# Kernel tuning notes

Measured on AMD Instinct MI355X. Metric: run time of the kernel, lower is better.

## Reference

```python
import jax, jax.numpy as jnp
import numpy as np

SCALE = 64.0
MARGIN = 0.35
EPS = 1e-7


def setup_inputs() -> dict:
    key = jax.random.key(0)
    k1, k2, k3 = jax.random.split(key, 3)
    B, D, C = 1024, 128, 100000
    embeddings = jax.random.normal(k1, (B, D), dtype=jnp.float32)
    labels = jax.random.randint(k2, (B,), 0, C, dtype=jnp.int64)
    W = jax.random.normal(k3, (C, D), dtype=jnp.float32)
    return {"embeddings": embeddings, "labels": labels, "W": W}


def reference(embeddings, labels, W):
    # L2-normalize class weights along feature dim (torch F.normalize, p=2, dim=1)
    W_norm = W / jnp.clip(jnp.linalg.norm(W, axis=1, keepdims=True), 1e-12)
    # cosine logits [B, C]
    cos_theta = jnp.clip(embeddings @ W_norm.T, -1.0 + EPS, 1.0 - EPS)
    # subtract margin only at the target class (equivalent to one-hot scatter)
    B = cos_theta.shape[0]
    rows = jnp.arange(B)
    cos_m = cos_theta.at[rows, labels].add(-MARGIN)
    logits = SCALE * cos_m
    # softmax cross-entropy with integer labels, mean reduction
    logp = jax.nn.log_softmax(logits, axis=-1)
    nll = -logp[rows, labels]
    return jnp.mean(nll)
```

## Files before the change

### kernel.cpp

```cpp
#include <hip/hip_runtime.h>
#include <hip/hip_bf16.h>

typedef __bf16 bf16x8 __attribute__((ext_vector_type(8)));
typedef float  f32x4  __attribute__((ext_vector_type(4)));

#define B_SZ 1024
#define D_SZ 128
#define C_SZ 100000
#define CPAD 100096
#define BM 128
#define BN 128
#define NG 64
#define NCT 782

#define SCALE_F   64.0f
#define MARGIN_F  0.35f
#define CLIP_F    (1.0f - 1e-7f)
#define LOG2E_F   1.4426950408889634f
#define S_LOG2E_F (64.0f * 1.4426950408889634f)

__device__ __forceinline__ void gload_lds16(const void* g, void* l) {
    __builtin_amdgcn_global_load_lds(
        (const __attribute__((address_space(1))) void*)g,
        (__attribute__((address_space(3))) void*)l, 16, 0, 0);
}

__global__ void norm_conv(const float* __restrict__ W, __bf16* __restrict__ Wb,
                          const float* __restrict__ E, __bf16* __restrict__ Eb) {
    const int b = blockIdx.x;
    if (b < 12512) {
        const int lane = threadIdx.x & 63;
        const int l32  = lane & 31;
        const int row  = b * 8 + ((threadIdx.x >> 6) << 1) + (lane >> 5);
        if (row < C_SZ) {
            float4 v = reinterpret_cast<const float4*>(W + (size_t)row * D_SZ)[l32];
            float ss = v.x * v.x + v.y * v.y + v.z * v.z + v.w * v.w;
            #pragma unroll
            for (int m = 1; m < 32; m <<= 1) ss += __shfl_xor(ss, m);
            float sc = 1.0f / fmaxf(sqrtf(ss), 1e-12f);
            union { __bf16 h[4]; uint2 u; } o;
            o.h[0] = (__bf16)(v.x * sc); o.h[1] = (__bf16)(v.y * sc);
            o.h[2] = (__bf16)(v.z * sc); o.h[3] = (__bf16)(v.w * sc);
            reinterpret_cast<uint2*>(Wb + (size_t)row * D_SZ)[l32] = o.u;
        } else {
            uint2 z; z.x = 0u; z.y = 0u;
            reinterpret_cast<uint2*>(Wb + (size_t)row * D_SZ)[l32] = z;
        }
    } else {
        const int i = (b - 12512) * 256 + threadIdx.x;
        float4 v = reinterpret_cast<const float4*>(E)[i];
        union { __bf16 h[4]; uint2 u; } o;
        o.h[0] = (__bf16)v.x; o.h[1] = (__bf16)v.y;
        o.h[2] = (__bf16)v.z; o.h[3] = (__bf16)v.w;
        reinterpret_cast<uint2*>(Eb)[i] = o.u;
    }
}

__launch_bounds__(512, 3)
__global__ void gemm_lse(const __bf16* __restrict__ Eb, const __bf16* __restrict__ Wb,
                         float* __restrict__ P) {
    __shared__ __bf16 sB[2][BN * D_SZ];
    __shared__ float  rs[2][BM];

    const int tid  = threadIdx.x;
    const int wave = tid >> 6;
    const int lane = tid & 63;
    const int g4   = lane >> 4;
    const int l15  = lane & 15;
    const int wm   = wave >> 1;
    const int wn   = wave & 1;
    const int g    = blockIdx.x;
    const int bi   = blockIdx.y;

    const int T = (NCT - g + NG - 1) / NG;

    const char* wbase = reinterpret_cast<const char*>(Wb);
    const int srcOff = ((tid >> 4) << 8) + ((((tid & 15) ^ ((tid >> 4) & 7))) << 4);
    const int ldsOff = wave << 10;

    {
        char* sb = reinterpret_cast<char*>(sB[0]);
        #pragma unroll
        for (int j = 0; j < 4; ++j)
            gload_lds16(wbase + (size_t)g * 32768 + j * 8192 + srcOff,
                        sb + j * 8192 + ldsOff);
    }

    bf16x8 a[2][4];
    {
        const char* ebase = reinterpret_cast<const char*>(Eb) + (size_t)bi * BM * 256;
        #pragma unroll
        for (int mi = 0; mi < 2; ++mi) {
            const char* pr = ebase + (wm * 32 + mi * 16 + l15) * 256 + g4 * 16;
            #pragma unroll
            for (int kk = 0; kk < 4; ++kk)
                a[mi][kk] = *reinterpret_cast<const bf16x8*>(pr + kk * 64);
        }
    }

    const int swz = (l15 & 7) << 4;
    int rowb[4];
    #pragma unroll
    for (int ni = 0; ni < 4; ++ni) rowb[ni] = (wn * 64 + ni * 16 + l15) * 256;
    int kb[4];
    #pragma unroll
    for (int kk = 0; kk < 4; ++kk) kb[kk] = (kk * 64 + g4 * 16) ^ swz;

    float rowsum[2][4] = {};

#define EPI(AC)                                                                  \
    _Pragma("unroll")                                                            \
    for (int mi = 0; mi < 2; ++mi) {                                             \
        _Pragma("unroll")                                                        \
        for (int r = 0; r < 4; ++r) {                                            \
            rowsum[mi][r] += __builtin_amdgcn_exp2f(                             \
                fminf(fmaf(AC[mi][0][r], S_LOG2E_F, -S_LOG2E_F), 0.0f));         \
            rowsum[mi][r] += __builtin_amdgcn_exp2f(                             \
                fminf(fmaf(AC[mi][1][r], S_LOG2E_F, -S_LOG2E_F), 0.0f));         \
        }                                                                        \
    }

    f32x4 acA[2][2], acB[2][2];
    #pragma unroll
    for (int mi = 0; mi < 2; ++mi)
        #pragma unroll
        for (int nh = 0; nh < 2; ++nh)
            acB[mi][nh] = (f32x4){0.f, 0.f, 0.f, 0.f};

    __syncthreads();

    int cur = 0;
    for (int t = 0; t < T; ++t) {
        if (t + 1 < T) {
            const size_t ci = (size_t)(g + (t + 1) * NG) * 32768;
            char* sb = reinterpret_cast<char*>(sB[cur ^ 1]);
            #pragma unroll
            for (int j = 0; j < 4; ++j)
                gload_lds16(wbase + ci + j * 8192 + srcOff, sb + j * 8192 + ldsOff);
        }

        const char* sBb = reinterpret_cast<const char*>(sB[cur]);

        __builtin_amdgcn_s_setprio(1);
        #pragma unroll
        for (int mi = 0; mi < 2; ++mi)
            #pragma unroll
            for (int nh = 0; nh < 2; ++nh)
                acA[mi][nh] = (f32x4){0.f, 0.f, 0.f, 0.f};
        #pragma unroll
        for (int kk = 0; kk < 4; ++kk) {
            bf16x8 b0 = *reinterpret_cast<const bf16x8*>(sBb + rowb[0] + kb[kk]);
            bf16x8 b1 = *reinterpret_cast<const bf16x8*>(sBb + rowb[1] + kb[kk]);
            acA[0][0] = __builtin_amdgcn_mfma_f32_16x16x32_bf16(a[0][kk], b0, acA[0][0], 0, 0, 0);
            acA[1][0] = __builtin_amdgcn_mfma_f32_16x16x32_bf16(a[1][kk], b0, acA[1][0], 0, 0, 0);
            acA[0][1] = __builtin_amdgcn_mfma_f32_16x16x32_bf16(a[0][kk], b1, acA[0][1], 0, 0, 0);
            acA[1][1] = __builtin_amdgcn_mfma_f32_16x16x32_bf16(a[1][kk], b1, acA[1][1], 0, 0, 0);
        }
        __builtin_amdgcn_s_setprio(0);
        EPI(acB);

        __builtin_amdgcn_s_setprio(1);
        #pragma unroll
        for (int mi = 0; mi < 2; ++mi)
            #pragma unroll
            for (int nh = 0; nh < 2; ++nh)
                acB[mi][nh] = (f32x4){0.f, 0.f, 0.f, 0.f};
        #pragma unroll
        for (int kk = 0; kk < 4; ++kk) {
            bf16x8 b2 = *reinterpret_cast<const bf16x8*>(sBb + rowb[2] + kb[kk]);
            bf16x8 b3 = *reinterpret_cast<const bf16x8*>(sBb + rowb[3] + kb[kk]);
            acB[0][0] = __builtin_amdgcn_mfma_f32_16x16x32_bf16(a[0][kk], b2, acB[0][0], 0, 0, 0);
            acB[1][0] = __builtin_amdgcn_mfma_f32_16x16x32_bf16(a[1][kk], b2, acB[1][0], 0, 0, 0);
            acB[0][1] = __builtin_amdgcn_mfma_f32_16x16x32_bf16(a[0][kk], b3, acB[0][1], 0, 0, 0);
            acB[1][1] = __builtin_amdgcn_mfma_f32_16x16x32_bf16(a[1][kk], b3, acB[1][1], 0, 0, 0);
        }
        __builtin_amdgcn_s_setprio(0);
        EPI(acA);

        __syncthreads();
        cur ^= 1;
    }
    EPI(acB);

    #pragma unroll
    for (int mi = 0; mi < 2; ++mi) {
        #pragma unroll
        for (int r = 0; r < 4; ++r) {
            float s = rowsum[mi][r];
            s += __shfl_xor(s, 1);
            s += __shfl_xor(s, 2);
            s += __shfl_xor(s, 4);
            s += __shfl_xor(s, 8);
            rowsum[mi][r] = s;
        }
    }
    if (l15 == 0) {
        #pragma unroll
        for (int mi = 0; mi < 2; ++mi)
            #pragma unroll
            for (int r = 0; r < 4; ++r)
                rs[wn][wm * 32 + mi * 16 + g4 * 4 + r] = rowsum[mi][r];
    }
    __syncthreads();
    if (tid < BM)
        P[(size_t)g * B_SZ + bi * BM + tid] = rs[0][tid] + rs[1][tid];
}

__global__ void row_fin(const float* __restrict__ P, const __bf16* __restrict__ Eb,
                        const __bf16* __restrict__ Wb, const int* __restrict__ lab,
                        float* __restrict__ nll) {
    __shared__ float red[256];
    const int row = blockIdx.x;
    const int t   = threadIdx.x;

    red[t] = (t < NG) ? P[(size_t)t * B_SZ + row] : 0.0f;
    __syncthreads();
    #pragma unroll
    for (int off = 128; off > 0; off >>= 1) {
        if (t < off) red[t] += red[t + off];
        __syncthreads();
    }
    const float S = red[0];
    __syncthreads();

    const int lb = lab[row];
    float d = 0.0f;
    if (t < 128) d = (float)Eb[row * D_SZ + t] * (float)Wb[(size_t)lb * D_SZ + t];
    red[t] = d;
    __syncthreads();
    #pragma unroll
    for (int off = 128; off > 0; off >>= 1) {
        if (t < off) red[t] += red[t + off];
        __syncthreads();
    }

    if (t == 0) {
        const float ct = red[0];
        const float cc = fminf(fmaxf(ct, -CLIP_F), CLIP_F);
        const float lt = SCALE_F * (cc - MARGIN_F);
        float Sadj = S - exp2f((SCALE_F * cc - SCALE_F) * LOG2E_F)
                       + exp2f((lt - SCALE_F) * LOG2E_F);
        nll[row] = SCALE_F + logf(Sadj) - lt;
    }
}

__global__ void mean_k(const float* __restrict__ nll, float* __restrict__ out) {
    __shared__ float part[16];
    const int t = threadIdx.x;
    float v = nll[t];
    #pragma unroll
    for (int m = 1; m < 64; m <<= 1) v += __shfl_xor(v, m);
    if ((t & 63) == 0) part[t >> 6] = v;
    __syncthreads();
    if (t < 16) {
        float u = part[t];
        #pragma unroll
        for (int m = 1; m < 16; m <<= 1) u += __shfl_xor(u, m);
        if (t == 0) out[0] = u * (1.0f / 1024.0f);
    }
}

extern "C" void kernel_launch(void* const* d_in, const int* in_sizes, int n_in,
                              void* d_out, int out_size, void* d_ws, size_t ws_size,
                              hipStream_t stream) {
    const float* E   = (const float*)d_in[0];
    const int*   lab = (const int*)d_in[1];
    const float* W   = (const float*)d_in[2];
    float*       out = (float*)d_out;

    char* ws = (char*)d_ws;
    __bf16* Eb  = (__bf16*)ws;
    __bf16* Wb  = (__bf16*)(ws + 262144);
    float*  P   = (float*)(ws + 262144 + 25624576);
    float*  nll = (float*)(ws + 262144 + 25624576 + 262144);

    norm_conv<<<dim3(12640),   256, 0, stream>>>(W, Wb, E, Eb);
    gemm_lse <<<dim3(NG, 8),   512, 0, stream>>>(Eb, Wb, P);
    row_fin  <<<dim3(B_SZ),    256, 0, stream>>>(P, Eb, Wb, lab, nll);
    mean_k   <<<dim3(1),      1024, 0, stream>>>(nll, out);
}
```

Before: 56.86 us.

## Halve GEMM class tile to 64 and drop software-pipelined epilogue interleave

Shrinks the class-dimension tile of the fused GEMM+logsumexp kernel from 128 to 64 columns, doubling the number of column groups (NG 64→128) and grid blocks. It also removes the two-accumulator ping-pong that overlapped the exp epilogue of one half-tile with the MFMAs of the other, along with the setprio hints, replacing it with a single accumulator set followed by a plain epilogue. Smaller LDS use allows a higher occupancy target of 4 blocks per CU. The partial buffer doubles in size, so the nll workspace offset moves. The trade is more blocks and occupancy in exchange for losing the intra-wave MFMA/exp overlap and paying one barrier per 64 columns instead of per 128.

Measured after the change: 60.84 us. 7.0% more time.

```diff
diff --git a/kernel.cpp b/kernel.cpp
--- a/kernel.cpp
+++ b/kernel.cpp
@@ -9,9 +9,9 @@
 #define C_SZ 100000
 #define CPAD 100096
 #define BM 128
-#define BN 128
-#define NG 64
-#define NCT 782
+#define BN 64
+#define NG 128
+#define NCT 1564
 
 #define SCALE_F   64.0f
 #define MARGIN_F  0.35f
@@ -56,7 +56,7 @@
     }
 }
 
-__launch_bounds__(512, 3)
+__launch_bounds__(512, 4)
 __global__ void gemm_lse(const __bf16* __restrict__ Eb, const __bf16* __restrict__ Wb,
                          float* __restrict__ P) {
     __shared__ __bf16 sB[2][BN * D_SZ];
@@ -81,8 +81,8 @@
     {
         char* sb = reinterpret_cast<char*>(sB[0]);
         #pragma unroll
-        for (int j = 0; j < 4; ++j)
-            gload_lds16(wbase + (size_t)g * 32768 + j * 8192 + srcOff,
+        for (int j = 0; j < 2; ++j)
+            gload_lds16(wbase + (size_t)g * 16384 + j * 8192 + srcOff,
                         sb + j * 8192 + ldsOff);
     }
 
@@ -99,88 +99,53 @@
     }
 
     const int swz = (l15 & 7) << 4;
-    int rowb[4];
-    #pragma unroll
-    for (int ni = 0; ni < 4; ++ni) rowb[ni] = (wn * 64 + ni * 16 + l15) * 256;
+    int rowb[2];
+    #pragma unroll
+    for (int ni = 0; ni < 2; ++ni) rowb[ni] = (wn * 32 + ni * 16 + l15) * 256;
     int kb[4];
     #pragma unroll
     for (int kk = 0; kk < 4; ++kk) kb[kk] = (kk * 64 + g4 * 16) ^ swz;
 
     float rowsum[2][4] = {};
-
-#define EPI(AC)                                                                  \
-    _Pragma("unroll")                                                            \
-    for (int mi = 0; mi < 2; ++mi) {                                             \
-        _Pragma("unroll")                                                        \
-        for (int r = 0; r < 4; ++r) {                                            \
-            rowsum[mi][r] += __builtin_amdgcn_exp2f(                             \
-                fminf(fmaf(AC[mi][0][r], S_LOG2E_F, -S_LOG2E_F), 0.0f));         \
-            rowsum[mi][r] += __builtin_amdgcn_exp2f(                             \
-                fminf(fmaf(AC[mi][1][r], S_LOG2E_F, -S_LOG2E_F), 0.0f));         \
-        }                                                                        \
-    }
-
-    f32x4 acA[2][2], acB[2][2];
-    #pragma unroll
-    for (int mi = 0; mi < 2; ++mi)
-        #pragma unroll
-        for (int nh = 0; nh < 2; ++nh)
-            acB[mi][nh] = (f32x4){0.f, 0.f, 0.f, 0.f};
 
     __syncthreads();
 
     int cur = 0;
     for (int t = 0; t < T; ++t) {
         if (t + 1 < T) {
-            const size_t ci = (size_t)(g + (t + 1) * NG) * 32768;
+            const size_t ci = (size_t)(g + (t + 1) * NG) * 16384;
             char* sb = reinterpret_cast<char*>(sB[cur ^ 1]);
             #pragma unroll
-            for (int j = 0; j < 4; ++j)
+            for (int j = 0; j < 2; ++j)
                 gload_lds16(wbase + ci + j * 8192 + srcOff, sb + j * 8192 + ldsOff);
         }
 
         const char* sBb = reinterpret_cast<const char*>(sB[cur]);
-
-        __builtin_amdgcn_s_setprio(1);
-        #pragma unroll
-        for (int mi = 0; mi < 2; ++mi)
-            #pragma unroll
-            for (int nh = 0; nh < 2; ++nh)
-                acA[mi][nh] = (f32x4){0.f, 0.f, 0.f, 0.f};
+        f32x4 acc[2][2] = {};
         #pragma unroll
         for (int kk = 0; kk < 4; ++kk) {
             bf16x8 b0 = *reinterpret_cast<const bf16x8*>(sBb + rowb[0] + kb[kk]);
             bf16x8 b1 = *reinterpret_cast<const bf16x8*>(sBb + rowb[1] + kb[kk]);
-            acA[0][0] = __builtin_amdgcn_mfma_f32_16x16x32_bf16(a[0][kk], b0, acA[0][0], 0, 0, 0);
-            acA[1][0] = __builtin_amdgcn_mfma_f32_16x16x32_bf16(a[1][kk], b0, acA[1][0], 0, 0, 0);
-            acA[0][1] = __builtin_amdgcn_mfma_f32_16x16x32_bf16(a[0][kk], b1, acA[0][1], 0, 0, 0);
-            acA[1][1] = __builtin_amdgcn_mfma_f32_16x16x32_bf16(a[1][kk], b1, acA[1][1], 0, 0, 0);
-        }
-        __builtin_amdgcn_s_setprio(0);
-        EPI(acB);
-
-        __builtin_amdgcn_s_setprio(1);
-        #pragma unroll
-        for (int mi = 0; mi < 2; ++mi)
-            #pragma unroll
-            for (int nh = 0; nh < 2; ++nh)
-                acB[mi][nh] = (f32x4){0.f, 0.f, 0.f, 0.f};
-        #pragma unroll
-        for (int kk = 0; kk < 4; ++kk) {
-            bf16x8 b2 = *reinterpret_cast<const bf16x8*>(sBb + rowb[2] + kb[kk]);
-            bf16x8 b3 = *reinterpret_cast<const bf16x8*>(sBb + rowb[3] + kb[kk]);
-            acB[0][0] = __builtin_amdgcn_mfma_f32_16x16x32_bf16(a[0][kk], b2, acB[0][0], 0, 0, 0);
-            acB[1][0] = __builtin_amdgcn_mfma_f32_16x16x32_bf16(a[1][kk], b2, acB[1][0], 0, 0, 0);
-            acB[0][1] = __builtin_amdgcn_mfma_f32_16x16x32_bf16(a[0][kk], b3, acB[0][1], 0, 0, 0);
-            acB[1][1] = __builtin_amdgcn_mfma_f32_16x16x32_bf16(a[1][kk], b3, acB[1][1], 0, 0, 0);
-        }
-        __builtin_amdgcn_s_setprio(0);
-        EPI(acA);
-
+            acc[0][0] = __builtin_amdgcn_mfma_f32_16x16x32_bf16(a[0][kk], b0, acc[0][0], 0, 0, 0);
+            acc[1][0] = __builtin_amdgcn_mfma_f32_16x16x32_bf16(a[1][kk], b0, acc[1][0], 0, 0, 0);
+            acc[0][1] = __builtin_amdgcn_mfma_f32_16x16x32_bf16(a[0][kk], b1, acc[0][1], 0, 0, 0);
+            acc[1][1] = __builtin_amdgcn_mfma_f32_16x16x32_bf16(a[1][kk], b1, acc[1][1], 0, 0, 0);
+        }
+
+        #pragma unroll
+        for (int mi = 0; mi < 2; ++mi) {
+            #pragma unroll
+            for (int r = 0; r < 4; ++r) {
+                float s0 = __builtin_amdgcn_exp2f(
+                    fminf(fmaf(acc[mi][0][r], S_LOG2E_F, -S_LOG2E_F), 0.0f));
+                float s1 = __builtin_amdgcn_exp2f(
+                    fminf(fmaf(acc[mi][1][r], S_LOG2E_F, -S_LOG2E_F), 0.0f));
+                rowsum[mi][r] += s0 + s1;
+            }
+        }
         __syncthreads();
         cur ^= 1;
     }
-    EPI(acB);
 
     #pragma unroll
     for (int mi = 0; mi < 2; ++mi) {
@@ -272,7 +237,7 @@
     __bf16* Eb  = (__bf16*)ws;
     __bf16* Wb  = (__bf16*)(ws + 262144);
     float*  P   = (float*)(ws + 262144 + 25624576);
-    float*  nll = (float*)(ws + 262144 + 25624576 + 262144);
+    float*  nll = (float*)(ws + 262144 + 25624576 + 524288);
 
     norm_conv<<<dim3(12640),   256, 0, stream>>>(W, Wb, E, Eb);
     gemm_lse <<<dim3(NG, 8),   512, 0, stream>>>(Eb, Wb, P);
```
